# Performance work log

Hardware: AMD Instinct MI355X
Metric: run time of the kernel (lower is better)

The kernel has to match this reference:

```python
import jax, jax.numpy as jnp
import numpy as np

H = 2048      # hidden_dim
P = 256       # private_subspace_dim
B, S = 4, 8192


def setup_inputs() -> dict:
    key = jax.random.key(0)
    k1, k2, k3, k4, k5 = jax.random.split(key, 5)
    hidden_states = jax.random.normal(k1, (B, S, H), dtype=jnp.float32)
    token_ids = jax.random.randint(k2, (B, S), 0, 100, dtype=jnp.int32)
    # Linear params (torch nn.Linear: y = x @ W.T + b); store W as (in, out) for einsum.
    sc1 = 1.0 / np.sqrt(H)
    sc2 = 1.0 / np.sqrt(P)
    W_to = jax.random.uniform(k3, (H, P), jnp.float32, -sc1, sc1)
    b_to = jnp.zeros((P,), jnp.float32)
    W_from = jax.random.uniform(k4, (P, H), jnp.float32, -sc2, sc2)
    b_from = jnp.zeros((H,), jnp.float32)
    return {
        "hidden_states": hidden_states,
        "W_to": W_to, "b_to": b_to,
        "W_from": W_from, "b_from": b_from,
        "token_ids": token_ids,
        "thought_token_id": 5,
    }


def _thought_mask(token_ids, thought_token_id):
    # Replaces the sequential toggle loop: state at position i is the parity of the
    # number of thought tokens seen in token_ids[0, :i+1] (toggle happens BEFORE use).
    matches = (token_ids[0] == thought_token_id).astype(jnp.int32)   # (S,)
    parity = (jnp.cumsum(matches) % 2) == 1                          # (S,) bool
    return jnp.broadcast_to(parity[None, :], token_ids.shape)        # (B, S)


def reference(hidden_states, W_to, b_to, W_from, b_from, token_ids, thought_token_id):
    is_private = _thought_mask(token_ids, thought_token_id)          # (B, S) bool
    m = is_private.astype(hidden_states.dtype)[..., None]            # (B, S, 1)
    private_reasoning = jnp.einsum('bsh,hp->bsp', hidden_states, W_to) + b_to
    private_projected = jnp.einsum('bsp,ph->bsh', private_reasoning, W_from) + b_from
    output = hidden_states * (1.0 - m) + private_projected * m
    subspace_usage = is_private.astype(jnp.float32).mean(axis=1)     # (B,)
    return private_reasoning, output, is_private, subspace_usage
```

## Files before the change

### kernel.cpp

```cpp
#include <hip/hip_runtime.h>
#include <stdint.h>


#define H 2048
#define P 256
#define BB 4
#define S 8192
#define M_TOTAL (BB * S)

typedef __bf16 bf16x8 __attribute__((ext_vector_type(8)));
typedef float f32x4 __attribute__((ext_vector_type(4)));

typedef const __attribute__((address_space(1))) uint32_t* gas_ptr;
typedef __attribute__((address_space(3))) uint32_t* las_ptr;

__device__ __forceinline__ void gload16(const ushort* g, ushort* l) {
  __builtin_amdgcn_global_load_lds((gas_ptr)g, (las_ptr)l, 16, 0, 0);
}

__device__ __forceinline__ ushort f2b(float f) {
  uint32_t u = __float_as_uint(f);
  u += 0x7fffu + ((u >> 16) & 1u);
  return (ushort)(u >> 16);
}

__global__ __launch_bounds__(256) void prep(
    const float* __restrict__ W_to, const float* __restrict__ W_from,
    ushort* __restrict__ wtT, ushort* __restrict__ wfT,
    const int* __restrict__ tok, const int* __restrict__ tt_p,
    float* __restrict__ maskf, int* __restrict__ slist, int* __restrict__ cntp,
    float* __restrict__ out2, float* __restrict__ out3) {
  __shared__ float tile[32][33];
  __shared__ unsigned long long wpar[4];
  __shared__ int scnt[256];
  const int b = blockIdx.x;
  const int t = threadIdx.x;
  if (b < 1024) {
    const float* in = (b < 512) ? W_to : W_from;
    ushort* out = (b < 512) ? wtT : wfT;
    const int R = (b < 512) ? H : P;
    const int C = (b < 512) ? P : H;
    const int bb = b & 511;
    const int nct = C >> 5;
    const int c0 = (bb % nct) * 32, r0 = (bb / nct) * 32;
    const int tx = t & 31, ty = t >> 5;
#pragma unroll
    for (int j = 0; j < 32; j += 8)
      tile[ty + j][tx] = in[(size_t)(r0 + ty + j) * C + c0 + tx];
    __syncthreads();
#pragma unroll
    for (int j = 0; j < 32; j += 8)
      out[(size_t)(c0 + ty + j) * R + r0 + tx] = f2b(tile[tx][ty + j]);
  } else {
    const int lane = t & 63, w = t >> 6;
    const int tt = tt_p[0];
    const int base = t * 32;
    unsigned bits = 0;
    for (int i = 0; i < 32; i++) bits |= (unsigned)(tok[base + i] == tt) << i;
    const int par = __popc(bits) & 1;
    const unsigned long long bal = __ballot(par != 0);
    if (lane == 0) wpar[w] = bal;
    __syncthreads();
    int pre = 0;
    for (int j = 0; j < w; j++) pre ^= (int)(__popcll(wpar[j]) & 1);
    pre ^= (int)(__popcll(bal & ((1ull << lane) - 1ull)) & 1);
    int cnt = 0;
    for (int i = 0; i < 32; i++) {
      int inc = __popc(bits << (31 - i)) & 1;
      cnt += pre ^ inc;
    }
    scnt[t] = cnt;
    __syncthreads();
    int off = 0, tot = 0;
    for (int j = 0; j < 256; j++) {
      if (j < t) off += scnt[j];
      tot += scnt[j];
    }
    for (int i = 0; i < 32; i++) {
      int inc = __popc(bits << (31 - i)) & 1;
      int bit = pre ^ inc;
      float fb = (float)bit;
      maskf[base + i] = fb;
      out2[0 * S + base + i] = fb;
      out2[1 * S + base + i] = fb;
      out2[2 * S + base + i] = fb;
      out2[3 * S + base + i] = fb;
      if (bit) slist[off++] = base + i;
    }
    const int padded = (tot + 127) & ~127;
    for (int idx = tot + t; idx < padded; idx += 256) slist[idx] = -1;
    if (t == 0) cntp[0] = tot;
    if (t < BB) out3[t] = (float)tot / (float)S;
  }
}

__global__ __launch_bounds__(512, 8) void gemm1(
    const float* __restrict__ hid,
    const ushort* __restrict__ wtT,
    const float* __restrict__ b_to,
    const float* __restrict__ maskf,
    float* __restrict__ out0,
    float* __restrict__ out1)
{
  __shared__ __align__(16) ushort sA[32 * 72];
  __shared__ __align__(16) ushort sW[256 * 64];
  const int tid = threadIdx.x;
  const int lane = tid & 63, wid = tid >> 6;
  const int quad = lane >> 4, l16 = lane & 15;
  const int swz = (l16 & 7) << 3;
  const int row0 = blockIdx.x * 32;

  const int grow = lane >> 3;
  const int kx = (((lane & 7) ^ (grow & 7)) << 3);
  const ushort* wSrcBase = wtT + (size_t)(wid * 32 + grow) * H + kx;
  ushort* wDstBase = sW + wid * 4 * 512;

  const int ra = tid >> 4, cc = tid & 15;
  const bool pass0 = (maskf[(row0 + ra) & (S - 1)] == 0.0f);
  const float* aSrc0 = hid + (size_t)(row0 + ra) * H + cc * 4;
  float* pDst0 = out1 + (size_t)(row0 + ra) * H + cc * 4;

  f32x4 acc[2][2];
  const f32x4 zero = {0.f, 0.f, 0.f, 0.f};
#pragma unroll
  for (int i = 0; i < 2; i++)
#pragma unroll
    for (int j = 0; j < 2; j++) acc[i][j] = zero;

  for (int k0 = 0; k0 < H; k0 += 64) {
#pragma unroll
    for (int j = 0; j < 4; j++)
      gload16(wSrcBase + (size_t)(8 * j) * H + k0, wDstBase + j * 512);
    {
      const float4 v0 = *(const float4*)(aSrc0 + k0);
      ushort4 b0;
      b0.x = f2b(v0.x); b0.y = f2b(v0.y); b0.z = f2b(v0.z); b0.w = f2b(v0.w);
      *(ushort4*)(sA + ra * 72 + cc * 4) = b0;
      if (pass0) *(float4*)(pDst0 + k0) = v0;
    }
    __syncthreads();
#pragma unroll
    for (int kk = 0; kk < 64; kk += 32) {
      bf16x8 af[2], bfr[2];
#pragma unroll
      for (int t = 0; t < 2; t++)
        af[t] = *(const bf16x8*)(sA + (t * 16 + l16) * 72 + kk + quad * 8);
#pragma unroll
      for (int t = 0; t < 2; t++)
        bfr[t] = *(const bf16x8*)(sW + (wid * 32 + t * 16 + l16) * 64 + ((kk + quad * 8) ^ swz));
#pragma unroll
      for (int i = 0; i < 2; i++)
#pragma unroll
        for (int j = 0; j < 2; j++)
          acc[i][j] = __builtin_amdgcn_mfma_f32_16x16x32_bf16(af[i], bfr[j], acc[i][j], 0, 0, 0);
    }
    __syncthreads();
  }

#pragma unroll
  for (int i = 0; i < 2; i++) {
#pragma unroll
    for (int j = 0; j < 2; j++) {
      int col = wid * 32 + j * 16 + l16;
      float bias = b_to[col];
#pragma unroll
      for (int e = 0; e < 4; e++) {
        int row = i * 16 + quad * 4 + e;
        out0[(size_t)(row0 + row) * P + col] = acc[i][j][e] + bias;
      }
    }
  }
}

__global__ __launch_bounds__(512) void gemm2(
    const float* __restrict__ pr,
    const ushort* __restrict__ wfT,
    const float* __restrict__ b_from,
    const int* __restrict__ slist,
    const int* __restrict__ cntp,
    float* __restrict__ out1)
{
  __shared__ __align__(16) ushort sA[128 * 72];
  __shared__ __align__(16) ushort sW[128 * 64];
  __shared__ int sIdx[128];
  const int tid = threadIdx.x;

  const int cnt = cntp[0];
  const int tpb = (cnt + 127) >> 7;
  const int u0 = ((blockIdx.x & 7) << 9) + (blockIdx.x >> 3);
  const int mt = u0 >> 4;
  if (mt >= 4 * tpb) return;
  const int nt = u0 & 15;
  const int batch = mt / tpb, ms = mt - batch * tpb;
  const int nc0 = nt * 128;
  const size_t rbase = (size_t)batch * S;

  if (tid < 128) sIdx[tid] = slist[ms * 128 + tid];
  __syncthreads();

  const int lane = tid & 63, wid = tid >> 6;
  const int quad = lane >> 4, l16 = lane & 15;
  const int swz = (l16 & 7) << 3;
  const int wr = wid >> 1, wc = wid & 1;

  const int grow = lane >> 3;
  const int kx = (((lane & 7) ^ (grow & 7)) << 3);
  const ushort* wSrcBase = wfT + (size_t)(nc0 + wid * 16 + grow) * P + kx;
  ushort* wDstBase = sW + wid * 2 * 512;

  const int ra = tid >> 4, cc = tid & 15;
  const float* aSrc[4];
#pragma unroll
  for (int p = 0; p < 4; p++) {
    int sr = sIdx[ra + p * 32];
    int s = (sr < 0) ? 0 : sr;
    aSrc[p] = pr + (rbase + s) * P + cc * 4;
  }

  f32x4 acc[2][4];
  const f32x4 zero = {0.f, 0.f, 0.f, 0.f};
#pragma unroll
  for (int i = 0; i < 2; i++)
#pragma unroll
    for (int j = 0; j < 4; j++) acc[i][j] = zero;

  for (int k0 = 0; k0 < P; k0 += 64) {
#pragma unroll
    for (int j = 0; j < 2; j++)
      gload16(wSrcBase + (size_t)(8 * j) * P + k0, wDstBase + j * 512);
#pragma unroll
    for (int p = 0; p < 4; p++) {
      const float4 v = *(const float4*)(aSrc[p] + k0);
      ushort4 b;
      b.x = f2b(v.x); b.y = f2b(v.y); b.z = f2b(v.z); b.w = f2b(v.w);
      *(ushort4*)(sA + (p * 32 + ra) * 72 + cc * 4) = b;
    }
    __syncthreads();
#pragma unroll
    for (int kk = 0; kk < 64; kk += 32) {
      bf16x8 af[2], bfr[4];
#pragma unroll
      for (int t = 0; t < 2; t++)
        af[t] = *(const bf16x8*)(sA + (wr * 32 + t * 16 + l16) * 72 + kk + quad * 8);
#pragma unroll
      for (int t = 0; t < 4; t++)
        bfr[t] = *(const bf16x8*)(sW + (wc * 64 + t * 16 + l16) * 64 + ((kk + quad * 8) ^ swz));
#pragma unroll
      for (int i = 0; i < 2; i++)
#pragma unroll
        for (int j = 0; j < 4; j++)
          acc[i][j] = __builtin_amdgcn_mfma_f32_16x16x32_bf16(af[i], bfr[j], acc[i][j], 0, 0, 0);
    }
    __syncthreads();
  }

#pragma unroll
  for (int i = 0; i < 2; i++) {
#pragma unroll
    for (int e = 0; e < 4; e++) {
      int row = wr * 32 + i * 16 + quad * 4 + e;
      int sr = sIdx[row];
      if (sr >= 0) {
        size_t gr = rbase + sr;
#pragma unroll
        for (int j = 0; j < 4; j++) {
          int col = nc0 + wc * 64 + j * 16 + l16;
          out1[gr * H + col] = acc[i][j][e] + b_from[col];
        }
      }
    }
  }
}

extern "C" void kernel_launch(void* const* d_in, const int* in_sizes, int n_in,
                              void* d_out, int out_size, void* d_ws, size_t ws_size,
                              hipStream_t stream) {
  const float* hid    = (const float*)d_in[0];
  const float* W_to   = (const float*)d_in[1];
  const float* b_to   = (const float*)d_in[2];
  const float* W_from = (const float*)d_in[3];
  const float* b_from = (const float*)d_in[4];
  const int*   tok    = (const int*)d_in[5];
  const int*   tt     = (const int*)d_in[6];

  ushort* wtT = (ushort*)d_ws;
  ushort* wfT = wtT + (size_t)P * H;
  float* maskf = (float*)(wfT + (size_t)H * P);
  int* slist = (int*)(maskf + S);
  int* cntp = slist + S;

  float* out0 = (float*)d_out;
  float* out1 = out0 + (size_t)BB * S * P;
  float* out2 = out1 + (size_t)BB * S * H;
  float* out3 = out2 + (size_t)BB * S;

  hipLaunchKernelGGL(prep, dim3(1025), dim3(256), 0, stream,
                     W_to, W_from, wtT, wfT, tok, tt, maskf, slist, cntp, out2, out3);
  hipLaunchKernelGGL(gemm1, dim3(M_TOTAL / 32), dim3(512), 0, stream,
                     hid, wtT, b_to, maskf, out0, out1);
  hipLaunchKernelGGL(gemm2, dim3((M_TOTAL / 128) * (H / 128)), dim3(512), 0, stream,
                     out0, wfT, b_from, slist, cntp, out1);
}
```

Measured before the change: 626.1 us.

## Rewrite gemm1 without LDS: each wave computes 16 rows by full P from registers

gemm1 drops shared-memory staging and barriers. Each wave now owns 16 rows and all 256 output columns, loads A directly from global and converts it to bf16 in registers, and reads W fragments straight from global, which should hit in L2. This removes the __syncthreads and LDS traffic but makes every wave reread the full 1 MB bf16 W_to from cache. It also raises per-thread accumulator registers to 16 f32x4, with 64-row blocks of 256 threads.

```diff
diff --git a/kernel.cpp b/kernel.cpp
--- a/kernel.cpp
+++ b/kernel.cpp
@@ -8,6 +8,7 @@
 #define S 8192
 #define M_TOTAL (BB * S)
 
+typedef __bf16 bf16_t;
 typedef __bf16 bf16x8 __attribute__((ext_vector_type(8)));
 typedef float f32x4 __attribute__((ext_vector_type(4)));
 
@@ -94,7 +95,7 @@
   }
 }
 
-__global__ __launch_bounds__(512, 8) void gemm1(
+__global__ __launch_bounds__(256) void gemm1(
     const float* __restrict__ hid,
     const ushort* __restrict__ wtT,
     const float* __restrict__ b_to,
@@ -102,73 +103,48 @@
     float* __restrict__ out0,
     float* __restrict__ out1)
 {
-  __shared__ __align__(16) ushort sA[32 * 72];
-  __shared__ __align__(16) ushort sW[256 * 64];
   const int tid = threadIdx.x;
-  const int lane = tid & 63, wid = tid >> 6;
-  const int quad = lane >> 4, l16 = lane & 15;
-  const int swz = (l16 & 7) << 3;
-  const int row0 = blockIdx.x * 32;
-
-  const int grow = lane >> 3;
-  const int kx = (((lane & 7) ^ (grow & 7)) << 3);
-  const ushort* wSrcBase = wtT + (size_t)(wid * 32 + grow) * H + kx;
-  ushort* wDstBase = sW + wid * 4 * 512;
-
-  const int ra = tid >> 4, cc = tid & 15;
-  const bool pass0 = (maskf[(row0 + ra) & (S - 1)] == 0.0f);
-  const float* aSrc0 = hid + (size_t)(row0 + ra) * H + cc * 4;
-  float* pDst0 = out1 + (size_t)(row0 + ra) * H + cc * 4;
-
-  f32x4 acc[2][2];
+  const int lane = tid & 63;
+  const int wv = tid >> 6;
+  const int l16 = lane & 15, quad = lane >> 4;
+  const int rg = blockIdx.x * 4 + wv;
+  const int arow = rg * 16 + l16;
+  const bool pass = (maskf[arow & (S - 1)] == 0.0f);
+
+  const float* aPtr = hid + (size_t)arow * H + quad * 8;
+  float* pPtr = out1 + (size_t)arow * H + quad * 8;
+  const ushort* wPtr = wtT + (size_t)l16 * H + quad * 8;
+
+  f32x4 acc[16];
   const f32x4 zero = {0.f, 0.f, 0.f, 0.f};
 #pragma unroll
-  for (int i = 0; i < 2; i++)
-#pragma unroll
-    for (int j = 0; j < 2; j++) acc[i][j] = zero;
-
-  for (int k0 = 0; k0 < H; k0 += 64) {
-#pragma unroll
-    for (int j = 0; j < 4; j++)
-      gload16(wSrcBase + (size_t)(8 * j) * H + k0, wDstBase + j * 512);
-    {
-      const float4 v0 = *(const float4*)(aSrc0 + k0);
-      ushort4 b0;
-      b0.x = f2b(v0.x); b0.y = f2b(v0.y); b0.z = f2b(v0.z); b0.w = f2b(v0.w);
-      *(ushort4*)(sA + ra * 72 + cc * 4) = b0;
-      if (pass0) *(float4*)(pDst0 + k0) = v0;
-    }
-    __syncthreads();
-#pragma unroll
-    for (int kk = 0; kk < 64; kk += 32) {
-      bf16x8 af[2], bfr[2];
-#pragma unroll
-      for (int t = 0; t < 2; t++)
-        af[t] = *(const bf16x8*)(sA + (t * 16 + l16) * 72 + kk + quad * 8);
-#pragma unroll
-      for (int t = 0; t < 2; t++)
-        bfr[t] = *(const bf16x8*)(sW + (wid * 32 + t * 16 + l16) * 64 + ((kk + quad * 8) ^ swz));
-#pragma unroll
-      for (int i = 0; i < 2; i++)
-#pragma unroll
-        for (int j = 0; j < 2; j++)
-          acc[i][j] = __builtin_amdgcn_mfma_f32_16x16x32_bf16(af[i], bfr[j], acc[i][j], 0, 0, 0);
-    }
-    __syncthreads();
-  }
-
-#pragma unroll
-  for (int i = 0; i < 2; i++) {
-#pragma unroll
-    for (int j = 0; j < 2; j++) {
-      int col = wid * 32 + j * 16 + l16;
-      float bias = b_to[col];
-#pragma unroll
-      for (int e = 0; e < 4; e++) {
-        int row = i * 16 + quad * 4 + e;
-        out0[(size_t)(row0 + row) * P + col] = acc[i][j][e] + bias;
-      }
-    }
+  for (int j = 0; j < 16; ++j) acc[j] = zero;
+
+  for (int k0 = 0; k0 < H; k0 += 32) {
+    const float4 a0 = *(const float4*)(aPtr + k0);
+    const float4 a1 = *(const float4*)(aPtr + k0 + 4);
+    if (pass) {
+      *(float4*)(pPtr + k0) = a0;
+      *(float4*)(pPtr + k0 + 4) = a1;
+    }
+    bf16x8 af;
+    af[0] = (bf16_t)a0.x; af[1] = (bf16_t)a0.y; af[2] = (bf16_t)a0.z; af[3] = (bf16_t)a0.w;
+    af[4] = (bf16_t)a1.x; af[5] = (bf16_t)a1.y; af[6] = (bf16_t)a1.z; af[7] = (bf16_t)a1.w;
+#pragma unroll
+    for (int j = 0; j < 16; ++j) {
+      const bf16x8 bf = *(const bf16x8*)(wPtr + (size_t)j * 16 * H + k0);
+      acc[j] = __builtin_amdgcn_mfma_f32_16x16x32_bf16(af, bf, acc[j], 0, 0, 0);
+    }
+  }
+
+  const int orow0 = rg * 16 + quad * 4;
+#pragma unroll
+  for (int j = 0; j < 16; ++j) {
+    const int col = j * 16 + l16;
+    const float bias = b_to[col];
+#pragma unroll
+    for (int e = 0; e < 4; ++e)
+      out0[(size_t)(orow0 + e) * P + col] = acc[j][e] + bias;
   }
 }
 
@@ -296,7 +272,7 @@
 
   hipLaunchKernelGGL(prep, dim3(1025), dim3(256), 0, stream,
                      W_to, W_from, wtT, wfT, tok, tt, maskf, slist, cntp, out2, out3);
-  hipLaunchKernelGGL(gemm1, dim3(M_TOTAL / 32), dim3(512), 0, stream,
+  hipLaunchKernelGGL(gemm1, dim3(M_TOTAL / 64), dim3(256), 0, stream,
                      hid, wtT, b_to, maskf, out0, out1);
   hipLaunchKernelGGL(gemm2, dim3((M_TOTAL / 128) * (H / 128)), dim3(512), 0, stream,
                      out0, wfT, b_from, slist, cntp, out1);
```

New measurement: 814.4 us. +30.1%, slower.
